# Kernel optimization log

Hardware: AMD Instinct MI355X
Metric: run time of the kernel (lower is better)

Reference implementation:

```python
import jax, jax.numpy as jnp
import numpy as np
from jax import lax

DIM = 128
N_WORD = 10000
N_FP = 100000
WINDOW = 5
KS = 2 * WINDOW + 1
L_GNN = 3
L_CNN = 3
L_OUT = 2
B, N_ATOM, L_PROT = 64, 256, 2048


def setup_inputs() -> dict:
    key = jax.random.key(0)
    ks = jax.random.split(key, 20)
    s = 0.1  # weight scale (module uses a custom weights_init; any small init is fine)
    return {
        "fingerprints": jax.random.randint(ks[0], (B, N_ATOM), 0, N_FP),
        "adjacency": jax.random.uniform(ks[1], (B, N_ATOM, N_ATOM), jnp.float32),
        "words": jax.random.randint(ks[2], (B, L_PROT), 0, N_WORD),
        "cmask": jnp.ones((B, N_ATOM), jnp.float32),
        "pmask": jnp.ones((B, L_PROT), jnp.float32),
        "label": jax.random.normal(ks[3], (B, 1), jnp.float32),
        "emb_fp": jax.random.normal(ks[4], (N_FP, DIM), jnp.float32) * s,
        "emb_word": jax.random.normal(ks[5], (N_WORD, DIM), jnp.float32) * s,
        "Wg": jax.random.normal(ks[6], (L_GNN, DIM, DIM), jnp.float32) * s,
        "bg": jax.random.normal(ks[7], (L_GNN, DIM), jnp.float32) * s,
        "Wc": jax.random.normal(ks[8], (L_CNN, 1, 1, KS, KS), jnp.float32) * s,
        "bc": jax.random.normal(ks[9], (L_CNN,), jnp.float32) * s,
        "Wa": jax.random.normal(ks[10], (DIM, DIM), jnp.float32) * s,
        "ba": jax.random.normal(ks[11], (DIM,), jnp.float32) * s,
        "Wo": jax.random.normal(ks[12], (L_OUT, 2 * DIM, 2 * DIM), jnp.float32) * s,
        "bo": jax.random.normal(ks[13], (L_OUT, 2 * DIM), jnp.float32) * s,
        "Wi": jax.random.normal(ks[14], (1, 2 * DIM), jnp.float32) * s,
        "bi": jax.random.normal(ks[15], (1,), jnp.float32) * s,
    }


def _conv2d(x, k, b):
    # x: [B,1,L,D], k: [1,1,KS,KS] -> same-padded conv, scalar bias
    y = lax.conv_general_dilated(x, k, (1, 1), [(WINDOW, WINDOW), (WINDOW, WINDOW)],
                                 dimension_numbers=("NCHW", "OIHW", "NCHW"))
    return y + b


def reference(fingerprints, adjacency, words, cmask, pmask, label,
              emb_fp, emb_word, Wg, bg, Wc, bc, Wa, ba, Wo, bo, Wi, bi):
    # --- GNN over compound graph ---
    xs = emb_fp[fingerprints]                          # [B,N,D]
    for i in range(L_GNN):
        hs = jax.nn.relu(jnp.einsum("bnd,ed->bne", xs, Wg[i]) + bg[i])
        xs = xs + jnp.matmul(adjacency, hs)            # residual message passing
    cm = cmask[:, :, None]
    compound = jnp.sum(xs * cm, axis=1) / jnp.sum(cm, axis=1)   # [B,D]

    # --- attention-CNN over protein words ---
    wv = emb_word[words]                               # [B,L,D]
    x4 = wv[:, None, :, :]                             # [B,1,L,D]
    for i in range(L_CNN):
        x4 = jax.nn.relu(_conv2d(x4, Wc[i], bc[i]))
    xs_p = x4[:, 0]                                    # [B,L,D]
    h = jax.nn.relu(compound @ Wa.T + ba)              # [B,D]
    hs = jax.nn.relu(jnp.einsum("bld,ed->ble", xs_p, Wa) + ba)  # [B,L,D]
    weights = jnp.tanh(jnp.einsum("bld,bd->bl", hs, h))[:, :, None]  # [B,L,1]
    ys = weights * hs
    pm = pmask[:, :, None]
    protein = jnp.sum(ys * pm, axis=1) / jnp.sum(pm, axis=1)    # [B,D]

    # --- output head ---
    cat = jnp.concatenate([compound, protein], axis=1)  # [B,2D]
    for j in range(L_OUT):
        cat = jax.nn.relu(cat @ Wo[j].T + bo[j])
    affinity = cat @ Wi.T + bi                           # [B,1]
    loss = jnp.mean((affinity - label) ** 2)             # MSELoss, weight 1
    return (loss, affinity)
```

## Files before the change

kernel.cpp:

```cpp
#include <hip/hip_runtime.h>
#include <hip/hip_bf16.h>
#include <math.h>

#define DIM   128
#define NA    256
#define NB    64
#define LPROT 2048
#define KSZ   11

#define TROWS   64
#define NTILES  (LPROT / TROWS)
#define FRS     152
#define XRS     136
#define B0_ROWS 106
#define B1_ROWS 96

typedef __attribute__((ext_vector_type(8))) short short8v;
typedef __attribute__((ext_vector_type(4))) short short4v;
typedef __attribute__((ext_vector_type(4))) float float4v;

__device__ inline unsigned short f2bf(float f) {
  __hip_bfloat16 h = __float2bfloat16(f);
  unsigned short u; __builtin_memcpy(&u, &h, 2); return u;
}
__device__ inline float bf2f(unsigned short s) {
  union { unsigned u; float f; } v; v.u = ((unsigned)s) << 16;
  return v.f;
}

#define GSTR 256
#define HSTR 512
#define WSTR 256
__device__ inline int xsa(int n, int cb) { return (n * GSTR + cb) ^ ((n & 7) << 4); }
__device__ inline int hta(int e, int nb) { return (e * HSTR + nb) ^ ((e & 7) << 4); }
__device__ inline int wga(int e, int cb) { return (e * WSTR + cb) ^ ((e & 7) << 4); }

__global__ __launch_bounds__(512, 2) void k_gnn(const int* __restrict__ fp,
                                                const float* __restrict__ emb,
                                                const float* __restrict__ A,
                                                const float* __restrict__ Wg,
                                                const float* __restrict__ bg,
                                                const float* __restrict__ cmask,
                                                const float* __restrict__ Wa,
                                                const float* __restrict__ ba,
                                                float* __restrict__ compound,
                                                float* __restrict__ hv) {
  __shared__ __align__(16) char pool[65536 + 32768 + 4096 + 640];
  char* reg0 = pool;
  char* wgp  = pool + 65536;
  float* cred = (float*)(pool + 98304);
  float* comp = (float*)(pool + 98304 + 4096);
  float* scsp = (float*)(pool + 98304 + 4096 + 512);

  const int b = blockIdx.x;
  const int tid = threadIdx.x, lane = tid & 63, w = tid >> 6;
  const int lj = lane & 15, g = lane >> 4;
  const int rbase = w * 32;

  float4v xsacc[2][8];
  {
    int frow[2][4];
    #pragma unroll
    for (int m = 0; m < 2; ++m)
      #pragma unroll
      for (int jj = 0; jj < 4; ++jj)
        frow[m][jj] = fp[b * NA + rbase + m * 16 + g * 4 + jj];
    #pragma unroll
    for (int m = 0; m < 2; ++m)
      #pragma unroll
      for (int c = 0; c < 8; ++c)
        #pragma unroll
        for (int jj = 0; jj < 4; ++jj)
          xsacc[m][c][jj] = emb[(long)frow[m][jj] * DIM + c * 16 + lj];
  }

  #pragma unroll 1
  for (int lp = 0; lp < 3; ++lp) {
    __syncthreads();

    const float* Wgl = Wg + lp * DIM * DIM;
    for (int i = tid; i < 128 * 16; i += 512) {
      int row = i >> 4, c8 = (i & 15) * 8;
      float4 v0 = *(const float4*)&Wgl[row * DIM + c8];
      float4 v1 = *(const float4*)&Wgl[row * DIM + c8 + 4];
      short8v s;
      s[0] = (short)f2bf(v0.x); s[1] = (short)f2bf(v0.y);
      s[2] = (short)f2bf(v0.z); s[3] = (short)f2bf(v0.w);
      s[4] = (short)f2bf(v1.x); s[5] = (short)f2bf(v1.y);
      s[6] = (short)f2bf(v1.z); s[7] = (short)f2bf(v1.w);
      *(short8v*)(wgp + wga(row, c8 * 2)) = s;
    }

    #pragma unroll
    for (int m = 0; m < 2; ++m) {
      #pragma unroll
      for (int jj = 0; jj < 4; ++jj) {
        int r = rbase + m * 16 + g * 4 + jj;
        #pragma unroll
        for (int c = 0; c < 8; ++c)
          *(unsigned short*)(reg0 + xsa(r, (c * 16 + lj) * 2)) =
              f2bf(xsacc[m][c][jj]);
      }
    }
    __syncthreads();

    float4v hacc[2][8];
    #pragma unroll
    for (int m = 0; m < 2; ++m)
      #pragma unroll
      for (int c = 0; c < 8; ++c) hacc[m][c] = (float4v){0.f, 0.f, 0.f, 0.f};
    #pragma unroll
    for (int ks = 0; ks < 4; ++ks) {
      short8v a0 = *(const short8v*)(reg0 + xsa(rbase + lj,      ks * 64 + g * 16));
      short8v a1 = *(const short8v*)(reg0 + xsa(rbase + 16 + lj, ks * 64 + g * 16));
      #pragma unroll
      for (int c = 0; c < 8; ++c) {
        short8v bf = *(const short8v*)(wgp + wga(c * 16 + lj, ks * 64 + g * 16));
        hacc[0][c] = __builtin_amdgcn_mfma_f32_16x16x32_bf16(a0, bf, hacc[0][c], 0, 0, 0);
        hacc[1][c] = __builtin_amdgcn_mfma_f32_16x16x32_bf16(a1, bf, hacc[1][c], 0, 0, 0);
      }
    }
    __syncthreads();

    #pragma unroll
    for (int m = 0; m < 2; ++m) {
      int n0 = rbase + m * 16 + g * 4;
      #pragma unroll
      for (int c = 0; c < 8; ++c) {
        int e = c * 16 + lj;
        float bias = bg[lp * DIM + e];
        short4v s;
        #pragma unroll
        for (int jj = 0; jj < 4; ++jj)
          s[jj] = (short)f2bf(fmaxf(hacc[m][c][jj] + bias, 0.f));
        *(short4v*)(reg0 + hta(e, n0 * 2)) = s;
      }
    }
    __syncthreads();

    #pragma unroll 1
    for (int ks = 0; ks < 8; ++ks) {
      short8v af[2];
      #pragma unroll
      for (int m = 0; m < 2; ++m) {
        const float* p = &A[((long)b * NA + rbase + m * 16 + lj) * NA + ks * 32 + g * 8];
        float4 x = *(const float4*)p, y = *(const float4*)(p + 4);
        short8v t;
        t[0] = (short)f2bf(x.x); t[1] = (short)f2bf(x.y);
        t[2] = (short)f2bf(x.z); t[3] = (short)f2bf(x.w);
        t[4] = (short)f2bf(y.x); t[5] = (short)f2bf(y.y);
        t[6] = (short)f2bf(y.z); t[7] = (short)f2bf(y.w);
        af[m] = t;
      }
      #pragma unroll
      for (int c = 0; c < 8; ++c) {
        short8v bf = *(const short8v*)(reg0 + hta(c * 16 + lj, ks * 64 + g * 16));
        xsacc[0][c] = __builtin_amdgcn_mfma_f32_16x16x32_bf16(af[0], bf, xsacc[0][c], 0, 0, 0);
        xsacc[1][c] = __builtin_amdgcn_mfma_f32_16x16x32_bf16(af[1], bf, xsacc[1][c], 0, 0, 0);
      }
    }
  }
  __syncthreads();

  {
    float cm[2][4];
    #pragma unroll
    for (int m = 0; m < 2; ++m)
      #pragma unroll
      for (int jj = 0; jj < 4; ++jj)
        cm[m][jj] = cmask[b * NA + rbase + m * 16 + g * 4 + jj];
    #pragma unroll
    for (int c = 0; c < 8; ++c) {
      float p = 0.f;
      #pragma unroll
      for (int m = 0; m < 2; ++m)
        #pragma unroll
        for (int jj = 0; jj < 4; ++jj)
          p = fmaf(xsacc[m][c][jj], cm[m][jj], p);
      p += __shfl_xor(p, 16);
      p += __shfl_xor(p, 32);
      if (g == 0) cred[w * DIM + c * 16 + lj] = p;
    }
    if (w == 0) {
      float s = 0.f;
      for (int i = lane; i < NA; i += 64) s += cmask[b * NA + i];
      #pragma unroll
      for (int o = 32; o > 0; o >>= 1) s += __shfl_xor(s, o);
      if (lane == 0) scsp[0] = s;
    }
  }
  __syncthreads();
  if (tid < DIM) {
    float s = 0.f;
    #pragma unroll
    for (int ww = 0; ww < 8; ++ww) s += cred[ww * DIM + tid];
    float c = s / scsp[0];
    compound[b * DIM + tid] = c;
    comp[tid] = c;
  }
  __syncthreads();
  if (tid < DIM) {
    float acc = 0.f;
    for (int d = 0; d < DIM; d += 4) {
      float4 wv = *(const float4*)&Wa[tid * DIM + d];
      float4 x  = *(const float4*)&comp[d];
      acc = fmaf(x.x, wv.x, fmaf(x.y, wv.y, fmaf(x.z, wv.z, fmaf(x.w, wv.w, acc))));
    }
    hv[b * DIM + tid] = fmaxf(acc + ba[tid], 0.f);
  }
}

template <int N_RC, bool ROWCHK, bool BF16OUT>
__device__ inline void conv_fp8(const char* __restrict__ src, char* __restrict__ dst,
                                unsigned short* __restrict__ dstX,
                                const long* bfr, float bias, int dstart,
                                int lane, int cc) {
  const int lj = lane & 15, k0 = (lane >> 4) * 8;
  const int acol = 8 + cc * 16 + k0;
  for (int rc = 0; rc < N_RC; ++rc) {
    float4v acc = {0.f, 0.f, 0.f, 0.f};
    #pragma unroll
    for (int ki = 0; ki < KSZ; ++ki) {
      int srow = rc * 16 + lj + ki;
      long a = *(const long*)(src + srow * FRS + acol);
      acc = __builtin_amdgcn_mfma_f32_16x16x32_fp8_fp8(a, bfr[ki], acc, 0, 0, 0);
    }
    int orow = rc * 16 + (lane >> 4) * 4;
    int ocol = cc * 16 + lj;
    #pragma unroll
    for (int jj = 0; jj < 4; ++jj) {
      float v = fmaxf(acc[jj] + bias, 0.f);
      if constexpr (BF16OUT) {
        dstX[(orow + jj) * XRS + ocol] = f2bf(v);
      } else {
        char sv = 0;
        if (!ROWCHK || (unsigned)(dstart + orow + jj) < LPROT) {
          int p = __builtin_amdgcn_cvt_pk_fp8_f32(v, 0.f, 0, false);
          sv = (char)p;
        }
        dst[(orow + jj) * FRS + 8 + ocol] = sv;
      }
    }
  }
}

__global__ __launch_bounds__(512, 6) void k_protein(const int* __restrict__ words,
                                                    const float* __restrict__ emb_word,
                                                    const float* __restrict__ Wc,
                                                    const float* __restrict__ bc,
                                                    const float* __restrict__ Wa,
                                                    const float* __restrict__ ba,
                                                    const float* __restrict__ hvec,
                                                    const float* __restrict__ pmask,
                                                    float* __restrict__ prot_part) {
  __shared__ __align__(16) char pool[50752];
  char* buf0 = pool;
  char* buf1 = pool + 16128;
  unsigned short* bufX = (unsigned short*)(pool + 30720);
  float* wpad = (float*)(pool + 48128);
  float* h_s  = (float*)(pool + 50240);
  float* wpart = (float*)(pool + 16128);
  float* w_l   = (float*)(pool + 16128 + 2048);
  float* red   = (float*)(pool + 16128 + 2304);

  const int tile = blockIdx.x, b = blockIdx.y;
  const int r0   = tile * TROWS;
  const int tid  = threadIdx.x;
  const int lane = tid & 63, wave = tid >> 6;
  const int lj   = lane & 15;
  const int k0   = (lane >> 4) * 8;
  const int cc   = wave;

  {
    int4 z = {0, 0, 0, 0};
    int4* p0 = (int4*)pool;
    for (int i = tid; i < 30720 / 16; i += 512) p0[i] = z;
  }
  if (tid < DIM) h_s[tid] = hvec[b * DIM + tid];
  __syncthreads();

  for (int idx = tid; idx < B0_ROWS * 32; idx += 512) {
    int rloc = idx >> 5, c4 = idx & 31;
    int rg = r0 - 15 + rloc;
    if (rg >= 0 && rg < LPROT) {
      int w = words[b * LPROT + rg];
      float4 v = ((const float4*)(emb_word + (long)w * DIM))[c4];
      int p = __builtin_amdgcn_cvt_pk_fp8_f32(v.x, v.y, 0, false);
      p = __builtin_amdgcn_cvt_pk_fp8_f32(v.z, v.w, p, true);
      *(int*)(buf0 + rloc * FRS + 8 + c4 * 4) = p;
    }
  }

  const int bbase = 15 + k0 - lj;

  #pragma unroll 1
  for (int lp = 0; lp < 3; ++lp) {
    __syncthreads();
    for (int i = tid; i < KSZ * 48; i += 512) wpad[i] = 0.f;
    __syncthreads();
    if (tid < KSZ * KSZ) wpad[(tid / KSZ) * 48 + 18 + tid % KSZ] = Wc[lp * KSZ * KSZ + tid];
    __syncthreads();

    long bfr[KSZ];
    #pragma unroll
    for (int ki = 0; ki < KSZ; ++ki) {
      const float* wr = wpad + ki * 48 + bbase;
      int lo = __builtin_amdgcn_cvt_pk_fp8_f32(wr[0], wr[1], 0, false);
      lo = __builtin_amdgcn_cvt_pk_fp8_f32(wr[2], wr[3], lo, true);
      int hi = __builtin_amdgcn_cvt_pk_fp8_f32(wr[4], wr[5], 0, false);
      hi = __builtin_amdgcn_cvt_pk_fp8_f32(wr[6], wr[7], hi, true);
      bfr[ki] = ((long)hi << 32) | (unsigned)lo;
    }
    float bias = bc[lp];

    if (lp == 0)
      conv_fp8<6, true, false>(buf0, buf1, nullptr, bfr, bias, r0 - 10, lane, cc);
    else if (lp == 1)
      conv_fp8<5, true, false>(buf1, buf0, nullptr, bfr, bias, r0 - 5, lane, cc);
    else
      conv_fp8<4, false, true>(buf0, nullptr, bufX, bfr, bias, r0, lane, cc);
  }
  __syncthreads();

  {
    const char* xb = (const char*)bufX;
    float4v acc[4];
    #pragma unroll
    for (int rc = 0; rc < 4; ++rc) acc[rc] = (float4v){0.f, 0.f, 0.f, 0.f};
    #pragma unroll
    for (int ks = 0; ks < 4; ++ks) {
      const float* wrow = Wa + (cc * 16 + lj) * DIM + ks * 32 + k0;
      float4 wa = *(const float4*)wrow;
      float4 wb = *(const float4*)(wrow + 4);
      short8v bf;
      bf[0] = (short)f2bf(wa.x); bf[1] = (short)f2bf(wa.y);
      bf[2] = (short)f2bf(wa.z); bf[3] = (short)f2bf(wa.w);
      bf[4] = (short)f2bf(wb.x); bf[5] = (short)f2bf(wb.y);
      bf[6] = (short)f2bf(wb.z); bf[7] = (short)f2bf(wb.w);
      #pragma unroll
      for (int rc = 0; rc < 4; ++rc) {
        short8v a = *(const short8v*)(xb + (rc * 16 + lj) * (XRS * 2) + (ks * 32 + k0) * 2);
        acc[rc] = __builtin_amdgcn_mfma_f32_16x16x32_bf16(a, bf, acc[rc], 0, 0, 0);
      }
    }
    __syncthreads();
    float bav = ba[cc * 16 + lj];
    #pragma unroll
    for (int rc = 0; rc < 4; ++rc) {
      int orow = rc * 16 + (lane >> 4) * 4;
      int ocol = cc * 16 + lj;
      #pragma unroll
      for (int jj = 0; jj < 4; ++jj) {
        float v = fmaxf(acc[rc][jj] + bav, 0.f);
        bufX[(orow + jj) * XRS + ocol] = f2bf(v);
      }
    }
  }
  __syncthreads();

  {
    int l = tid >> 3, part = tid & 7, d0 = part * 16;
    float s = 0.f;
    #pragma unroll
    for (int dd = 0; dd < 16; ++dd)
      s = fmaf(bf2f(bufX[l * XRS + d0 + dd]), h_s[d0 + dd], s);
    wpart[l * 8 + part] = s;
  }
  __syncthreads();
  if (tid < TROWS) {
    float s = 0.f;
    #pragma unroll
    for (int p = 0; p < 8; ++p) s += wpart[tid * 8 + p];
    w_l[tid] = tanhf(s) * pmask[b * LPROT + r0 + tid];
  }
  __syncthreads();

  {
    int e = tid & 127, g = tid >> 7;
    float s = 0.f;
    #pragma unroll
    for (int j = 0; j < 16; ++j) {
      int l = g * 16 + j;
      s = fmaf(w_l[l], bf2f(bufX[l * XRS + e]), s);
    }
    red[g * DIM + e] = s;
  }
  __syncthreads();
  if (tid < DIM)
    prot_part[((long)b * NTILES + tile) * DIM + tid] =
        red[tid] + red[DIM + tid] + red[2 * DIM + tid] + red[3 * DIM + tid];
}

__global__ __launch_bounds__(256) void k_head(const float* __restrict__ prot_part,
                                              const float* __restrict__ pmask,
                                              const float* __restrict__ compound,
                                              const float* __restrict__ Wo,
                                              const float* __restrict__ bo,
                                              const float* __restrict__ Wi,
                                              const float* __restrict__ bi,
                                              float* __restrict__ out) {
  int b = blockIdx.x, tid = threadIdx.x;
  __shared__ float cat[2 * DIM];
  __shared__ float redl[256];

  float ps = 0.f;
  for (int l = tid; l < LPROT; l += 256) ps += pmask[b * LPROT + l];
  redl[tid] = ps; __syncthreads();
  for (int st = 128; st > 0; st >>= 1) {
    if (tid < st) redl[tid] += redl[tid + st];
    __syncthreads();
  }
  float pden = redl[0];
  __syncthreads();

  if (tid < DIM) {
    cat[tid] = compound[b * DIM + tid];
    float s = 0.f;
    for (int t = 0; t < NTILES; ++t) s += prot_part[(b * NTILES + t) * DIM + tid];
    cat[DIM + tid] = s / pden;
  }
  __syncthreads();

  for (int j = 0; j < 2; ++j) {
    const float* W = Wo + j * 2 * DIM * 2 * DIM + tid * 2 * DIM;
    float acc = 0.f;
    for (int d = 0; d < 2 * DIM; d += 4) {
      float4 c = *(const float4*)&cat[d];
      float4 w = *(const float4*)&W[d];
      acc = fmaf(c.x, w.x, fmaf(c.y, w.y, fmaf(c.z, w.z, fmaf(c.w, w.w, acc))));
    }
    float v = fmaxf(acc + bo[j * 2 * DIM + tid], 0.f);
    __syncthreads();
    cat[tid] = v;
    __syncthreads();
  }

  float p = cat[tid] * Wi[tid];
  redl[tid] = p; __syncthreads();
  for (int st = 128; st > 0; st >>= 1) {
    if (tid < st) redl[tid] += redl[tid + st];
    __syncthreads();
  }
  if (tid == 0) out[1 + b] = redl[0] + bi[0];
}

__global__ void k_loss(const float* __restrict__ label, float* __restrict__ out) {
  int t = threadIdx.x;
  float d = out[1 + t] - label[t];
  float v = d * d;
  #pragma unroll
  for (int s = 32; s > 0; s >>= 1) v += __shfl_down(v, s);
  if (t == 0) out[0] = v * (1.f / 64.f);
}

extern "C" void kernel_launch(void* const* d_in, const int* in_sizes, int n_in,
                              void* d_out, int out_size, void* d_ws, size_t ws_size,
                              hipStream_t stream) {
  const int*   fingerprints = (const int*)d_in[0];
  const float* adjacency    = (const float*)d_in[1];
  const int*   words        = (const int*)d_in[2];
  const float* cmask        = (const float*)d_in[3];
  const float* pmask        = (const float*)d_in[4];
  const float* label        = (const float*)d_in[5];
  const float* emb_fp       = (const float*)d_in[6];
  const float* emb_word     = (const float*)d_in[7];
  const float* Wg           = (const float*)d_in[8];
  const float* bg           = (const float*)d_in[9];
  const float* Wc           = (const float*)d_in[10];
  const float* bc           = (const float*)d_in[11];
  const float* Wa           = (const float*)d_in[12];
  const float* ba           = (const float*)d_in[13];
  const float* Wo           = (const float*)d_in[14];
  const float* bo           = (const float*)d_in[15];
  const float* Wi           = (const float*)d_in[16];
  const float* bi           = (const float*)d_in[17];
  float* out = (float*)d_out;

  float* ws        = (float*)d_ws;
  float* compound  = ws;
  float* hv        = compound + NB * DIM;
  float* prot_part = hv + NB * DIM;

  k_gnn<<<NB, 512, 0, stream>>>(fingerprints, emb_fp, adjacency, Wg, bg,
                                cmask, Wa, ba, compound, hv);
  k_protein<<<dim3(NTILES, NB), 512, 0, stream>>>(words, emb_word, Wc, bc, Wa, ba,
                                                  hv, pmask, prot_part);
  k_head<<<NB, 256, 0, stream>>>(prot_part, pmask, compound, Wo, bo, Wi, bi, out);
  k_loss<<<1, 64, 0, stream>>>(label, out);
}
```

Before: 156.5 us.

## Split fused GNN kernel into per-layer launches with 4 blocks per graph

Replaces the single 64-block GNN kernel, which ran all three layers per batch element, with three per-layer launches of 256 blocks each. Every block recomputes the full hs = relu(xs Wg + b) for its graph but only computes a 64-row quarter of the adjacency matmul. The intermediate xs is stored in fp32 in global workspace between layers. The compound mean and the Wa projection move to a separate small kernel. The aim is to occupy more of the GPU's compute units, at the price of redundant hs computation, extra global traffic for xs, and more kernel launches.

```diff
diff --git a/kernel.cpp b/kernel.cpp
--- a/kernel.cpp
+++ b/kernel.cpp
@@ -27,187 +27,180 @@
   union { unsigned u; float f; } v; v.u = ((unsigned)s) << 16;
   return v.f;
 }
-
-#define GSTR 256
+__device__ inline short8v cvt8(const float* p) {
+  float4 x = *(const float4*)p, y = *(const float4*)(p + 4);
+  short8v t;
+  t[0] = (short)f2bf(x.x); t[1] = (short)f2bf(x.y);
+  t[2] = (short)f2bf(x.z); t[3] = (short)f2bf(x.w);
+  t[4] = (short)f2bf(y.x); t[5] = (short)f2bf(y.y);
+  t[6] = (short)f2bf(y.z); t[7] = (short)f2bf(y.w);
+  return t;
+}
+
 #define HSTR 512
-#define WSTR 256
-__device__ inline int xsa(int n, int cb) { return (n * GSTR + cb) ^ ((n & 7) << 4); }
 __device__ inline int hta(int e, int nb) { return (e * HSTR + nb) ^ ((e & 7) << 4); }
-__device__ inline int wga(int e, int cb) { return (e * WSTR + cb) ^ ((e & 7) << 4); }
-
-__global__ __launch_bounds__(512, 2) void k_gnn(const int* __restrict__ fp,
-                                                const float* __restrict__ emb,
-                                                const float* __restrict__ A,
-                                                const float* __restrict__ Wg,
-                                                const float* __restrict__ bg,
-                                                const float* __restrict__ cmask,
-                                                const float* __restrict__ Wa,
-                                                const float* __restrict__ ba,
-                                                float* __restrict__ compound,
-                                                float* __restrict__ hv) {
-  __shared__ __align__(16) char pool[65536 + 32768 + 4096 + 640];
-  char* reg0 = pool;
-  char* wgp  = pool + 65536;
-  float* cred = (float*)(pool + 98304);
-  float* comp = (float*)(pool + 98304 + 4096);
-  float* scsp = (float*)(pool + 98304 + 4096 + 512);
-
-  const int b = blockIdx.x;
+
+template <bool GATHER, bool LAST>
+__global__ __launch_bounds__(512, 2) void k_gnn_layer(
+    const float* __restrict__ xs_in,
+    const int* __restrict__ fp,
+    const float* __restrict__ emb,
+    const float* __restrict__ A,
+    const float* __restrict__ Wg,
+    const float* __restrict__ bg,
+    const float* __restrict__ cmask,
+    float* __restrict__ xs_out,
+    float* __restrict__ cred) {
+  __shared__ __align__(16) char hsT[128 * HSTR];
+  const int blk = blockIdx.x;
+  const int b = blk >> 2, q = blk & 3;
   const int tid = threadIdx.x, lane = tid & 63, w = tid >> 6;
   const int lj = lane & 15, g = lane >> 4;
-  const int rbase = w * 32;
-
-  float4v xsacc[2][8];
+  const int k0 = g * 8;
+
   {
-    int frow[2][4];
+    int frow[2];
+    if (GATHER) {
+      frow[0] = fp[b * NA + w * 32 + lj];
+      frow[1] = fp[b * NA + w * 32 + 16 + lj];
+    }
+    short8v afr[4][2];
+    #pragma unroll
+    for (int m = 0; m < 2; ++m) {
+      const float* src = GATHER ? &emb[(long)frow[m] * DIM]
+                                : &xs_in[((long)b * NA + w * 32 + m * 16 + lj) * DIM];
+      #pragma unroll
+      for (int ks = 0; ks < 4; ++ks)
+        afr[ks][m] = cvt8(src + ks * 32 + k0);
+    }
+
+    float4v hacc[2][8];
     #pragma unroll
     for (int m = 0; m < 2; ++m)
       #pragma unroll
-      for (int jj = 0; jj < 4; ++jj)
-        frow[m][jj] = fp[b * NA + rbase + m * 16 + g * 4 + jj];
-    #pragma unroll
-    for (int m = 0; m < 2; ++m)
-      #pragma unroll
-      for (int c = 0; c < 8; ++c)
-        #pragma unroll
-        for (int jj = 0; jj < 4; ++jj)
-          xsacc[m][c][jj] = emb[(long)frow[m][jj] * DIM + c * 16 + lj];
-  }
-
-  #pragma unroll 1
-  for (int lp = 0; lp < 3; ++lp) {
-    __syncthreads();
-
-    const float* Wgl = Wg + lp * DIM * DIM;
-    for (int i = tid; i < 128 * 16; i += 512) {
-      int row = i >> 4, c8 = (i & 15) * 8;
-      float4 v0 = *(const float4*)&Wgl[row * DIM + c8];
-      float4 v1 = *(const float4*)&Wgl[row * DIM + c8 + 4];
-      short8v s;
-      s[0] = (short)f2bf(v0.x); s[1] = (short)f2bf(v0.y);
-      s[2] = (short)f2bf(v0.z); s[3] = (short)f2bf(v0.w);
-      s[4] = (short)f2bf(v1.x); s[5] = (short)f2bf(v1.y);
-      s[6] = (short)f2bf(v1.z); s[7] = (short)f2bf(v1.w);
-      *(short8v*)(wgp + wga(row, c8 * 2)) = s;
-    }
+      for (int c = 0; c < 8; ++c) hacc[m][c] = (float4v){0.f, 0.f, 0.f, 0.f};
+
+    #pragma unroll
+    for (int ks = 0; ks < 4; ++ks)
+      #pragma unroll
+      for (int c = 0; c < 8; ++c) {
+        short8v bf = cvt8(&Wg[(c * 16 + lj) * DIM + ks * 32 + k0]);
+        hacc[0][c] = __builtin_amdgcn_mfma_f32_16x16x32_bf16(afr[ks][0], bf, hacc[0][c], 0, 0, 0);
+        hacc[1][c] = __builtin_amdgcn_mfma_f32_16x16x32_bf16(afr[ks][1], bf, hacc[1][c], 0, 0, 0);
+      }
 
     #pragma unroll
     for (int m = 0; m < 2; ++m) {
-      #pragma unroll
-      for (int jj = 0; jj < 4; ++jj) {
-        int r = rbase + m * 16 + g * 4 + jj;
-        #pragma unroll
-        for (int c = 0; c < 8; ++c)
-          *(unsigned short*)(reg0 + xsa(r, (c * 16 + lj) * 2)) =
-              f2bf(xsacc[m][c][jj]);
-      }
-    }
-    __syncthreads();
-
-    float4v hacc[2][8];
-    #pragma unroll
-    for (int m = 0; m < 2; ++m)
-      #pragma unroll
-      for (int c = 0; c < 8; ++c) hacc[m][c] = (float4v){0.f, 0.f, 0.f, 0.f};
-    #pragma unroll
-    for (int ks = 0; ks < 4; ++ks) {
-      short8v a0 = *(const short8v*)(reg0 + xsa(rbase + lj,      ks * 64 + g * 16));
-      short8v a1 = *(const short8v*)(reg0 + xsa(rbase + 16 + lj, ks * 64 + g * 16));
-      #pragma unroll
-      for (int c = 0; c < 8; ++c) {
-        short8v bf = *(const short8v*)(wgp + wga(c * 16 + lj, ks * 64 + g * 16));
-        hacc[0][c] = __builtin_amdgcn_mfma_f32_16x16x32_bf16(a0, bf, hacc[0][c], 0, 0, 0);
-        hacc[1][c] = __builtin_amdgcn_mfma_f32_16x16x32_bf16(a1, bf, hacc[1][c], 0, 0, 0);
-      }
-    }
-    __syncthreads();
-
-    #pragma unroll
-    for (int m = 0; m < 2; ++m) {
-      int n0 = rbase + m * 16 + g * 4;
+      int n0 = w * 32 + m * 16 + g * 4;
       #pragma unroll
       for (int c = 0; c < 8; ++c) {
         int e = c * 16 + lj;
-        float bias = bg[lp * DIM + e];
+        float bias = bg[e];
         short4v s;
         #pragma unroll
         for (int jj = 0; jj < 4; ++jj)
           s[jj] = (short)f2bf(fmaxf(hacc[m][c][jj] + bias, 0.f));
-        *(short4v*)(reg0 + hta(e, n0 * 2)) = s;
-      }
-    }
-    __syncthreads();
-
-    #pragma unroll 1
-    for (int ks = 0; ks < 8; ++ks) {
-      short8v af[2];
-      #pragma unroll
-      for (int m = 0; m < 2; ++m) {
-        const float* p = &A[((long)b * NA + rbase + m * 16 + lj) * NA + ks * 32 + g * 8];
-        float4 x = *(const float4*)p, y = *(const float4*)(p + 4);
-        short8v t;
-        t[0] = (short)f2bf(x.x); t[1] = (short)f2bf(x.y);
-        t[2] = (short)f2bf(x.z); t[3] = (short)f2bf(x.w);
-        t[4] = (short)f2bf(y.x); t[5] = (short)f2bf(y.y);
-        t[6] = (short)f2bf(y.z); t[7] = (short)f2bf(y.w);
-        af[m] = t;
-      }
-      #pragma unroll
-      for (int c = 0; c < 8; ++c) {
-        short8v bf = *(const short8v*)(reg0 + hta(c * 16 + lj, ks * 64 + g * 16));
-        xsacc[0][c] = __builtin_amdgcn_mfma_f32_16x16x32_bf16(af[0], bf, xsacc[0][c], 0, 0, 0);
-        xsacc[1][c] = __builtin_amdgcn_mfma_f32_16x16x32_bf16(af[1], bf, xsacc[1][c], 0, 0, 0);
-      }
-    }
-  }
-  __syncthreads();
-
-  {
-    float cm[2][4];
+        *(short4v*)(hsT + hta(e, n0 * 2)) = s;
+      }
+    }
+  }
+  __syncthreads();
+
+  const int wr = w >> 2, wc = w & 3;
+  const int row0 = q * 64 + wr * 32;
+
+  float4v acc[2][2];
+  #pragma unroll
+  for (int m = 0; m < 2; ++m)
+    #pragma unroll
+    for (int c = 0; c < 2; ++c) acc[m][c] = (float4v){0.f, 0.f, 0.f, 0.f};
+
+  #pragma unroll 2
+  for (int ks = 0; ks < 8; ++ks) {
+    short8v af[2];
     #pragma unroll
     for (int m = 0; m < 2; ++m)
-      #pragma unroll
-      for (int jj = 0; jj < 4; ++jj)
-        cm[m][jj] = cmask[b * NA + rbase + m * 16 + g * 4 + jj];
-    #pragma unroll
-    for (int c = 0; c < 8; ++c) {
-      float p = 0.f;
-      #pragma unroll
-      for (int m = 0; m < 2; ++m)
+      af[m] = cvt8(&A[((long)b * NA + row0 + m * 16 + lj) * NA + ks * 32 + k0]);
+    #pragma unroll
+    for (int c = 0; c < 2; ++c) {
+      short8v bf = *(const short8v*)(hsT + hta(wc * 32 + c * 16 + lj, (ks * 32 + k0) * 2));
+      acc[0][c] = __builtin_amdgcn_mfma_f32_16x16x32_bf16(af[0], bf, acc[0][c], 0, 0, 0);
+      acc[1][c] = __builtin_amdgcn_mfma_f32_16x16x32_bf16(af[1], bf, acc[1][c], 0, 0, 0);
+    }
+  }
+
+  if (!LAST) {
+    #pragma unroll
+    for (int m = 0; m < 2; ++m)
+      #pragma unroll
+      for (int jj = 0; jj < 4; ++jj) {
+        int row = row0 + m * 16 + g * 4 + jj;
+        long base = ((long)b * NA + row) * DIM;
+        const float* oldsrc;
+        long gbase = 0;
+        if (GATHER) { gbase = (long)fp[b * NA + row] * DIM; oldsrc = emb; }
+        else { gbase = base; oldsrc = xs_in; }
         #pragma unroll
-        for (int jj = 0; jj < 4; ++jj)
-          p = fmaf(xsacc[m][c][jj], cm[m][jj], p);
-      p += __shfl_xor(p, 16);
-      p += __shfl_xor(p, 32);
-      if (g == 0) cred[w * DIM + c * 16 + lj] = p;
-    }
-    if (w == 0) {
-      float s = 0.f;
-      for (int i = lane; i < NA; i += 64) s += cmask[b * NA + i];
-      #pragma unroll
-      for (int o = 32; o > 0; o >>= 1) s += __shfl_xor(s, o);
-      if (lane == 0) scsp[0] = s;
-    }
-  }
-  __syncthreads();
-  if (tid < DIM) {
-    float s = 0.f;
-    #pragma unroll
-    for (int ww = 0; ww < 8; ++ww) s += cred[ww * DIM + tid];
-    float c = s / scsp[0];
-    compound[b * DIM + tid] = c;
-    comp[tid] = c;
-  }
-  __syncthreads();
-  if (tid < DIM) {
-    float acc = 0.f;
-    for (int d = 0; d < DIM; d += 4) {
-      float4 wv = *(const float4*)&Wa[tid * DIM + d];
-      float4 x  = *(const float4*)&comp[d];
-      acc = fmaf(x.x, wv.x, fmaf(x.y, wv.y, fmaf(x.z, wv.z, fmaf(x.w, wv.w, acc))));
-    }
-    hv[b * DIM + tid] = fmaxf(acc + ba[tid], 0.f);
-  }
+        for (int c = 0; c < 2; ++c) {
+          int col = wc * 32 + c * 16 + lj;
+          xs_out[base + col] = oldsrc[gbase + col] + acc[m][c][jj];
+        }
+      }
+  } else {
+    float p[2] = {0.f, 0.f};
+    #pragma unroll
+    for (int m = 0; m < 2; ++m)
+      #pragma unroll
+      for (int jj = 0; jj < 4; ++jj) {
+        int row = row0 + m * 16 + g * 4 + jj;
+        float cm = cmask[b * NA + row];
+        long base = ((long)b * NA + row) * DIM;
+        #pragma unroll
+        for (int c = 0; c < 2; ++c) {
+          int col = wc * 32 + c * 16 + lj;
+          float xv = xs_in[base + col] + acc[m][c][jj];
+          p[c] = fmaf(xv, cm, p[c]);
+        }
+      }
+    #pragma unroll
+    for (int c = 0; c < 2; ++c) {
+      p[c] += __shfl_xor(p[c], 16);
+      p[c] += __shfl_xor(p[c], 32);
+      if (g == 0)
+        cred[((long)b * 8 + q * 2 + wr) * DIM + wc * 32 + c * 16 + lj] = p[c];
+    }
+  }
+}
+
+__global__ __launch_bounds__(128) void k_hv(const float* __restrict__ cred,
+                                            const float* __restrict__ cmask,
+                                            const float* __restrict__ Wa,
+                                            const float* __restrict__ ba,
+                                            float* __restrict__ compound,
+                                            float* __restrict__ hv) {
+  int b = blockIdx.x, e = threadIdx.x;
+  __shared__ float comp[DIM];
+  __shared__ float redm[DIM];
+  float s = 0.f;
+  #pragma unroll
+  for (int p = 0; p < 8; ++p) s += cred[((long)b * 8 + p) * DIM + e];
+  redm[e] = cmask[b * NA + e] + cmask[b * NA + DIM + e];
+  __syncthreads();
+  for (int st = 64; st > 0; st >>= 1) {
+    if (e < st) redm[e] += redm[e + st];
+    __syncthreads();
+  }
+  float c = s / redm[0];
+  compound[b * DIM + e] = c;
+  comp[e] = c;
+  __syncthreads();
+  float acc = 0.f;
+  for (int d = 0; d < DIM; d += 4) {
+    float4 wv = *(const float4*)&Wa[e * DIM + d];
+    float4 x  = *(const float4*)&comp[d];
+    acc = fmaf(x.x, wv.x, fmaf(x.y, wv.y, fmaf(x.z, wv.z, fmaf(x.w, wv.w, acc))));
+  }
+  hv[b * DIM + e] = fmaxf(acc + ba[e], 0.f);
 }
 
 template <int N_RC, bool ROWCHK, bool BF16OUT>
@@ -330,13 +323,7 @@
     #pragma unroll
     for (int ks = 0; ks < 4; ++ks) {
       const float* wrow = Wa + (cc * 16 + lj) * DIM + ks * 32 + k0;
-      float4 wa = *(const float4*)wrow;
-      float4 wb = *(const float4*)(wrow + 4);
-      short8v bf;
-      bf[0] = (short)f2bf(wa.x); bf[1] = (short)f2bf(wa.y);
-      bf[2] = (short)f2bf(wa.z); bf[3] = (short)f2bf(wa.w);
-      bf[4] = (short)f2bf(wb.x); bf[5] = (short)f2bf(wb.y);
-      bf[6] = (short)f2bf(wb.z); bf[7] = (short)f2bf(wb.w);
+      short8v bf = cvt8(wrow);
       #pragma unroll
       for (int rc = 0; rc < 4; ++rc) {
         short8v a = *(const short8v*)(xb + (rc * 16 + lj) * (XRS * 2) + (ks * 32 + k0) * 2);
@@ -477,12 +464,22 @@
   float* out = (float*)d_out;
 
   float* ws        = (float*)d_ws;
-  float* compound  = ws;
+  float* xs1       = ws;
+  float* xs2       = xs1 + NB * NA * DIM;
+  float* cred      = xs2 + NB * NA * DIM;
+  float* compound  = cred + NB * 8 * DIM;
   float* hv        = compound + NB * DIM;
   float* prot_part = hv + NB * DIM;
 
-  k_gnn<<<NB, 512, 0, stream>>>(fingerprints, emb_fp, adjacency, Wg, bg,
-                                cmask, Wa, ba, compound, hv);
+  k_gnn_layer<true,  false><<<NB * 4, 512, 0, stream>>>(
+      nullptr, fingerprints, emb_fp, adjacency, Wg, bg, nullptr, xs1, nullptr);
+  k_gnn_layer<false, false><<<NB * 4, 512, 0, stream>>>(
+      xs1, fingerprints, emb_fp, adjacency, Wg + DIM * DIM, bg + DIM,
+      nullptr, xs2, nullptr);
+  k_gnn_layer<false, true><<<NB * 4, 512, 0, stream>>>(
+      xs2, fingerprints, emb_fp, adjacency, Wg + 2 * DIM * DIM, bg + 2 * DIM,
+      cmask, nullptr, cred);
+  k_hv<<<NB, 128, 0, stream>>>(cred, cmask, Wa, ba, compound, hv);
   k_protein<<<dim3(NTILES, NB), 512, 0, stream>>>(words, emb_word, Wc, bc, Wa, ba,
                                                   hv, pmask, prot_part);
   k_head<<<NB, 256, 0, stream>>>(prot_part, pmask, compound, Wo, bo, Wi, bi, out);
```

New measurement: 198.4 us. 26.8% more time.

## Pre-convert adjacency to bf16 once, prefetch A fragments, pair conv row chunks

Applied to the files above, without the earlier changes.

A separate kernel now converts the adjacency matrix to bf16 in workspace a single time, instead of reloading and converting fp32 A in each of the three GNN layers. The GNN kernel then loads all A fragments for a layer before running its MFMA loop. The fp8 conv processes two row chunks per iteration for more MFMA independence, and the attention dot product uses vectorized LDS loads. The cost is an extra launch and an extra write and read of the bf16 adjacency, plus higher register pressure in the GNN kernel from the prefetched fragments.

```diff
diff --git a/kernel.cpp b/kernel.cpp
--- a/kernel.cpp
+++ b/kernel.cpp
@@ -27,6 +27,21 @@
   union { unsigned u; float f; } v; v.u = ((unsigned)s) << 16;
   return v.f;
 }
+__device__ inline short8v cvt8(const float* p) {
+  float4 x = *(const float4*)p, y = *(const float4*)(p + 4);
+  short8v t;
+  t[0] = (short)f2bf(x.x); t[1] = (short)f2bf(x.y);
+  t[2] = (short)f2bf(x.z); t[3] = (short)f2bf(x.w);
+  t[4] = (short)f2bf(y.x); t[5] = (short)f2bf(y.y);
+  t[6] = (short)f2bf(y.z); t[7] = (short)f2bf(y.w);
+  return t;
+}
+
+__global__ __launch_bounds__(256) void k_cvtA(const float* __restrict__ A,
+                                              unsigned short* __restrict__ Abf) {
+  long i = ((long)blockIdx.x * 256 + threadIdx.x) * 8;
+  *(short8v*)(Abf + i) = cvt8(A + i);
+}
 
 #define GSTR 256
 #define HSTR 512
@@ -37,7 +52,7 @@
 
 __global__ __launch_bounds__(512, 2) void k_gnn(const int* __restrict__ fp,
                                                 const float* __restrict__ emb,
-                                                const float* __restrict__ A,
+                                                const unsigned short* __restrict__ Abf,
                                                 const float* __restrict__ Wg,
                                                 const float* __restrict__ bg,
                                                 const float* __restrict__ cmask,
@@ -55,6 +70,7 @@
   const int b = blockIdx.x;
   const int tid = threadIdx.x, lane = tid & 63, w = tid >> 6;
   const int lj = lane & 15, g = lane >> 4;
+  const int k0 = g * 8;
   const int rbase = w * 32;
 
   float4v xsacc[2][8];
@@ -81,14 +97,7 @@
     const float* Wgl = Wg + lp * DIM * DIM;
     for (int i = tid; i < 128 * 16; i += 512) {
       int row = i >> 4, c8 = (i & 15) * 8;
-      float4 v0 = *(const float4*)&Wgl[row * DIM + c8];
-      float4 v1 = *(const float4*)&Wgl[row * DIM + c8 + 4];
-      short8v s;
-      s[0] = (short)f2bf(v0.x); s[1] = (short)f2bf(v0.y);
-      s[2] = (short)f2bf(v0.z); s[3] = (short)f2bf(v0.w);
-      s[4] = (short)f2bf(v1.x); s[5] = (short)f2bf(v1.y);
-      s[6] = (short)f2bf(v1.z); s[7] = (short)f2bf(v1.w);
-      *(short8v*)(wgp + wga(row, c8 * 2)) = s;
+      *(short8v*)(wgp + wga(row, c8 * 2)) = cvt8(&Wgl[row * DIM + c8]);
     }
 
     #pragma unroll
@@ -138,27 +147,21 @@
     }
     __syncthreads();
 
-    #pragma unroll 1
-    for (int ks = 0; ks < 8; ++ks) {
-      short8v af[2];
-      #pragma unroll
-      for (int m = 0; m < 2; ++m) {
-        const float* p = &A[((long)b * NA + rbase + m * 16 + lj) * NA + ks * 32 + g * 8];
-        float4 x = *(const float4*)p, y = *(const float4*)(p + 4);
-        short8v t;
-        t[0] = (short)f2bf(x.x); t[1] = (short)f2bf(x.y);
-        t[2] = (short)f2bf(x.z); t[3] = (short)f2bf(x.w);
-        t[4] = (short)f2bf(y.x); t[5] = (short)f2bf(y.y);
-        t[6] = (short)f2bf(y.z); t[7] = (short)f2bf(y.w);
-        af[m] = t;
-      }
+    short8v af[8][2];
+    #pragma unroll
+    for (int ks = 0; ks < 8; ++ks)
+      #pragma unroll
+      for (int m = 0; m < 2; ++m)
+        af[ks][m] = *(const short8v*)
+            &Abf[((long)b * NA + rbase + m * 16 + lj) * NA + ks * 32 + k0];
+    #pragma unroll
+    for (int ks = 0; ks < 8; ++ks)
       #pragma unroll
       for (int c = 0; c < 8; ++c) {
         short8v bf = *(const short8v*)(reg0 + hta(c * 16 + lj, ks * 64 + g * 16));
-        xsacc[0][c] = __builtin_amdgcn_mfma_f32_16x16x32_bf16(af[0], bf, xsacc[0][c], 0, 0, 0);
-        xsacc[1][c] = __builtin_amdgcn_mfma_f32_16x16x32_bf16(af[1], bf, xsacc[1][c], 0, 0, 0);
-      }
-    }
+        xsacc[0][c] = __builtin_amdgcn_mfma_f32_16x16x32_bf16(af[ks][0], bf, xsacc[0][c], 0, 0, 0);
+        xsacc[1][c] = __builtin_amdgcn_mfma_f32_16x16x32_bf16(af[ks][1], bf, xsacc[1][c], 0, 0, 0);
+      }
   }
   __syncthreads();
 
@@ -210,6 +213,30 @@
   }
 }
 
+template <bool ROWCHK, bool BF16OUT>
+__device__ inline void conv_epi(const float4v& acc, int rc,
+                                char* __restrict__ dst,
+                                unsigned short* __restrict__ dstX,
+                                float bias, int dstart, int lane, int cc) {
+  const int lj = lane & 15;
+  int orow = rc * 16 + (lane >> 4) * 4;
+  int ocol = cc * 16 + lj;
+  #pragma unroll
+  for (int jj = 0; jj < 4; ++jj) {
+    float v = fmaxf(acc[jj] + bias, 0.f);
+    if constexpr (BF16OUT) {
+      dstX[(orow + jj) * XRS + ocol] = f2bf(v);
+    } else {
+      char sv = 0;
+      if (!ROWCHK || (unsigned)(dstart + orow + jj) < LPROT) {
+        int p = __builtin_amdgcn_cvt_pk_fp8_f32(v, 0.f, 0, false);
+        sv = (char)p;
+      }
+      dst[(orow + jj) * FRS + 8 + ocol] = sv;
+    }
+  }
+}
+
 template <int N_RC, bool ROWCHK, bool BF16OUT>
 __device__ inline void conv_fp8(const char* __restrict__ src, char* __restrict__ dst,
                                 unsigned short* __restrict__ dstX,
@@ -217,30 +244,30 @@
                                 int lane, int cc) {
   const int lj = lane & 15, k0 = (lane >> 4) * 8;
   const int acol = 8 + cc * 16 + k0;
-  for (int rc = 0; rc < N_RC; ++rc) {
+  #pragma unroll 1
+  for (int rp = 0; rp < N_RC / 2; ++rp) {
+    const int rc0 = rp * 2, rc1 = rc0 + 1;
+    float4v acc0 = {0.f, 0.f, 0.f, 0.f};
+    float4v acc1 = {0.f, 0.f, 0.f, 0.f};
+    #pragma unroll
+    for (int ki = 0; ki < KSZ; ++ki) {
+      long a0 = *(const long*)(src + (rc0 * 16 + lj + ki) * FRS + acol);
+      long a1 = *(const long*)(src + (rc1 * 16 + lj + ki) * FRS + acol);
+      acc0 = __builtin_amdgcn_mfma_f32_16x16x32_fp8_fp8(a0, bfr[ki], acc0, 0, 0, 0);
+      acc1 = __builtin_amdgcn_mfma_f32_16x16x32_fp8_fp8(a1, bfr[ki], acc1, 0, 0, 0);
+    }
+    conv_epi<ROWCHK, BF16OUT>(acc0, rc0, dst, dstX, bias, dstart, lane, cc);
+    conv_epi<ROWCHK, BF16OUT>(acc1, rc1, dst, dstX, bias, dstart, lane, cc);
+  }
+  if (N_RC & 1) {
+    const int rc = N_RC - 1;
     float4v acc = {0.f, 0.f, 0.f, 0.f};
     #pragma unroll
     for (int ki = 0; ki < KSZ; ++ki) {
-      int srow = rc * 16 + lj + ki;
-      long a = *(const long*)(src + srow * FRS + acol);
+      long a = *(const long*)(src + (rc * 16 + lj + ki) * FRS + acol);
       acc = __builtin_amdgcn_mfma_f32_16x16x32_fp8_fp8(a, bfr[ki], acc, 0, 0, 0);
     }
-    int orow = rc * 16 + (lane >> 4) * 4;
-    int ocol = cc * 16 + lj;
-    #pragma unroll
-    for (int jj = 0; jj < 4; ++jj) {
-      float v = fmaxf(acc[jj] + bias, 0.f);
-      if constexpr (BF16OUT) {
-        dstX[(orow + jj) * XRS + ocol] = f2bf(v);
-      } else {
-        char sv = 0;
-        if (!ROWCHK || (unsigned)(dstart + orow + jj) < LPROT) {
-          int p = __builtin_amdgcn_cvt_pk_fp8_f32(v, 0.f, 0, false);
-          sv = (char)p;
-        }
-        dst[(orow + jj) * FRS + 8 + ocol] = sv;
-      }
-    }
+    conv_epi<ROWCHK, BF16OUT>(acc, rc, dst, dstX, bias, dstart, lane, cc);
   }
 }
 
@@ -330,13 +357,7 @@
     #pragma unroll
     for (int ks = 0; ks < 4; ++ks) {
       const float* wrow = Wa + (cc * 16 + lj) * DIM + ks * 32 + k0;
-      float4 wa = *(const float4*)wrow;
-      float4 wb = *(const float4*)(wrow + 4);
-      short8v bf;
-      bf[0] = (short)f2bf(wa.x); bf[1] = (short)f2bf(wa.y);
-      bf[2] = (short)f2bf(wa.z); bf[3] = (short)f2bf(wa.w);
-      bf[4] = (short)f2bf(wb.x); bf[5] = (short)f2bf(wb.y);
-      bf[6] = (short)f2bf(wb.z); bf[7] = (short)f2bf(wb.w);
+      short8v bf = cvt8(wrow);
       #pragma unroll
       for (int rc = 0; rc < 4; ++rc) {
         short8v a = *(const short8v*)(xb + (rc * 16 + lj) * (XRS * 2) + (ks * 32 + k0) * 2);
@@ -360,10 +381,29 @@
 
   {
     int l = tid >> 3, part = tid & 7, d0 = part * 16;
+    short8v v0 = *(const short8v*)&bufX[l * XRS + d0];
+    short8v v1 = *(const short8v*)&bufX[l * XRS + d0 + 8];
+    float4 h0 = *(const float4*)&h_s[d0];
+    float4 h1 = *(const float4*)&h_s[d0 + 4];
+    float4 h2 = *(const float4*)&h_s[d0 + 8];
+    float4 h3 = *(const float4*)&h_s[d0 + 12];
     float s = 0.f;
-    #pragma unroll
-    for (int dd = 0; dd < 16; ++dd)
-      s = fmaf(bf2f(bufX[l * XRS + d0 + dd]), h_s[d0 + dd], s);
+    s = fmaf(bf2f((unsigned short)v0[0]), h0.x, s);
+    s = fmaf(bf2f((unsigned short)v0[1]), h0.y, s);
+    s = fmaf(bf2f((unsigned short)v0[2]), h0.z, s);
+    s = fmaf(bf2f((unsigned short)v0[3]), h0.w, s);
+    s = fmaf(bf2f((unsigned short)v0[4]), h1.x, s);
+    s = fmaf(bf2f((unsigned short)v0[5]), h1.y, s);
+    s = fmaf(bf2f((unsigned short)v0[6]), h1.z, s);
+    s = fmaf(bf2f((unsigned short)v0[7]), h1.w, s);
+    s = fmaf(bf2f((unsigned short)v1[0]), h2.x, s);
+    s = fmaf(bf2f((unsigned short)v1[1]), h2.y, s);
+    s = fmaf(bf2f((unsigned short)v1[2]), h2.z, s);
+    s = fmaf(bf2f((unsigned short)v1[3]), h2.w, s);
+    s = fmaf(bf2f((unsigned short)v1[4]), h3.x, s);
+    s = fmaf(bf2f((unsigned short)v1[5]), h3.y, s);
+    s = fmaf(bf2f((unsigned short)v1[6]), h3.z, s);
+    s = fmaf(bf2f((unsigned short)v1[7]), h3.w, s);
     wpart[l * 8 + part] = s;
   }
   __syncthreads();
@@ -477,11 +517,13 @@
   float* out = (float*)d_out;
 
   float* ws        = (float*)d_ws;
-  float* compound  = ws;
+  unsigned short* Abf = (unsigned short*)ws;
+  float* compound  = (float*)(Abf + (long)NB * NA * NA);
   float* hv        = compound + NB * DIM;
   float* prot_part = hv + NB * DIM;
 
-  k_gnn<<<NB, 512, 0, stream>>>(fingerprints, emb_fp, adjacency, Wg, bg,
+  k_cvtA<<<(NB * NA * NA) / (256 * 8), 256, 0, stream>>>(adjacency, Abf);
+  k_gnn<<<NB, 512, 0, stream>>>(fingerprints, emb_fp, Abf, Wg, bg,
                                 cmask, Wa, ba, compound, hv);
   k_protein<<<dim3(NTILES, NB), 512, 0, stream>>>(words, emb_word, Wc, bc, Wa, ba,
                                                   hv, pmask, prot_part);
```

Measured after the change: 194.2 us. 1.24x slower.
